# Performance work log

Hardware: AMD Instinct MI355X
Metric: run time of the kernel (lower is better)

Reference implementation:

```python
import jax, jax.numpy as jnp
import numpy as np
from jax import lax

HMA = 8.0
H = W = 34
A = 15
IMH = IMW = 270.0
AW = jnp.array([9.232984,16.0,27.712813,18.465969,32.0,55.425626,36.931937,64.0,110.851252,73.863875,128.0,221.702503,147.72775,256.0,443.405007], jnp.float32)
AH = jnp.array([27.72668,16.0,9.237604,55.453359,32.0,18.475209,110.906719,64.0,36.950417,221.813438,128.0,73.900834,443.626876,256.0,147.801669], jnp.float32)
RPN_MEAN = jnp.array([0.000437,0.002586,-0.123953,-0.081469], jnp.float32)
RPN_STD = jnp.array([0.12677,0.095741,0.3173,0.281042], jnp.float32)
RCNN_STD = jnp.array([0.1,0.1,0.2,0.2], jnp.float32)
RPN_MIN = 6.16056
RCNN_MIN = 8.8008
NUM_CLASS = 3

def _decode(t, acx, acy, aw, ah):
    cx = t[..., 0] * aw + acx
    cy = t[..., 1] * ah + acy
    bw = jnp.exp(t[..., 2]) * aw
    bh = jnp.exp(t[..., 3]) * ah
    x1 = jnp.clip(cx - 0.5 * (bw - 1.0), 0.0, IMW - 1.0)
    y1 = jnp.clip(cy - 0.5 * (bh - 1.0), 0.0, IMH - 1.0)
    x2 = jnp.clip(cx + 0.5 * (bw - 1.0), 0.0, IMW - 1.0)
    y2 = jnp.clip(cy + 0.5 * (bh - 1.0), 0.0, IMH - 1.0)
    return jnp.stack([x1, y1, x2, y2], -1)

def _nms(boxes, scores, thresh, top_n):
    # greedy hard NMS, fixed top_n output with validity mask
    x1, y1, x2, y2 = boxes[:, 0], boxes[:, 1], boxes[:, 2], boxes[:, 3]
    areas = (x2 - x1 + 1.0) * (y2 - y1 + 1.0)
    n = boxes.shape[0]
    def step(scur, _):
        j = jnp.argmax(scur)
        valid = scur[j] > 0.0
        bj = boxes[j]
        iw = jnp.maximum(jnp.minimum(x2, bj[2]) - jnp.maximum(x1, bj[0]) + 1.0, 0.0)
        ih = jnp.maximum(jnp.minimum(y2, bj[3]) - jnp.maximum(y1, bj[1]) + 1.0, 0.0)
        inter = iw * ih
        iou = inter / (areas + areas[j] - inter)
        sup = (iou > thresh) | (jnp.arange(n) == j)
        return jnp.where(sup, -1.0, scur), (j, valid)
    _, (idx, valid) = lax.scan(step, scores, None, length=top_n)
    return idx, valid

def _psroi_one(ftr, roi):
    # ftr: [10,7,7,H,W] position-sensitive features; roi: [x1,y1,x2,y2] image coords
    sw = roi[0] / HMA; sh = roi[1] / HMA
    ew = (roi[2] + 1.0) / HMA; eh = (roi[3] + 1.0) / HMA
    rh = jnp.maximum(eh - sh, 0.1); rw = jnp.maximum(ew - sw, 0.1)
    bh = rh / 7.0; bw = rw / 7.0
    g = jnp.arange(7, dtype=jnp.float32); s = jnp.arange(4, dtype=jnp.float32)
    ys = sh + g[:, None] * bh + (s[None, :] + 0.5) * (bh / 4.0)  # [7(ph),4]
    xs = sw + g[:, None] * bw + (s[None, :] + 0.5) * (bw / 4.0)  # [7(pw),4]
    y0 = jnp.floor(ys); x0 = jnp.floor(xs)
    dy = ys - y0; dx = xs - x0
    y0i = y0.astype(jnp.int32); x0i = x0.astype(jnp.int32)
    c = jnp.arange(10)[:, None, None, None, None]
    P = jnp.arange(7)[None, :, None, None, None]
    Q = jnp.arange(7)[None, None, :, None, None]
    def corner(yi, xi, wy, wx):
        my = ((yi >= 0) & (yi < H)).astype(jnp.float32)
        mx = ((xi >= 0) & (xi < W)).astype(jnp.float32)
        yc = jnp.clip(yi, 0, H - 1); xc = jnp.clip(xi, 0, W - 1)
        v = ftr[c, P, Q, yc[None, :, None, :, None], xc[None, None, :, None, :]]
        return v * (wy * my)[None, :, None, :, None] * (wx * mx)[None, None, :, None, :]
    val = (corner(y0i, x0i, 1 - dy, 1 - dx) + corner(y0i, x0i + 1, 1 - dy, dx)
         + corner(y0i + 1, x0i, dy, 1 - dx) + corner(y0i + 1, x0i + 1, dy, dx))
    return val.mean(axis=(3, 4))  # [10,7,7]

def reference(rpn_cls_prob_reshape, rpn_bbox_pred, ft_add_left_right, W_inner, b_inner, W_cls, b_cls, W_bbox, b_bbox):
    # ---------- RPNProposalSSD ----------
    fg = rpn_cls_prob_reshape[0, A:, :, :].reshape(-1)  # [A*H*W] fg probs
    t = rpn_bbox_pred[0].reshape(A, 4, H, W).transpose(0, 2, 3, 1)  # [A,H,W,4]
    t = t * RPN_STD + RPN_MEAN
    acx = (jnp.arange(W, dtype=jnp.float32) * HMA)[None, None, :]
    acy = (jnp.arange(H, dtype=jnp.float32) * HMA)[None, :, None]
    boxes = _decode(t, acx, acy, AW[:, None, None], AH[:, None, None]).reshape(-1, 4)
    bw = boxes[:, 2] - boxes[:, 0] + 1.0; bh = boxes[:, 3] - boxes[:, 1] + 1.0
    keep = (fg >= 0.2) & ((bw >= RPN_MIN) | (bh >= RPN_MIN))
    top_s, top_i = lax.top_k(jnp.where(keep, fg, -1.0), 3000)
    cand = boxes[top_i]
    idx, valid = _nms(cand, top_s, 0.7, 300)
    vm = valid.astype(jnp.float32)[:, None]
    rois_xy = cand[idx] * vm  # [300,4], padded rows zeroed
    rois = jnp.concatenate([jnp.zeros((300, 1), jnp.float32), rois_xy], axis=1)
    rpn_scores = top_s[idx][:, None] * vm  # [300,1]
    # ---------- DFMBPSROIAlign ----------
    ftr = ft_add_left_right[0].reshape(10, 7, 7, H, W)
    pooled = jax.vmap(lambda r: _psroi_one(ftr, r))(rois_xy)  # [300,10,7,7]
    # ---------- FC head ----------
    feat = jax.nn.relu(pooled.reshape(-1, 490) @ W_inner.T + b_inner)
    probs = jax.nn.softmax(feat @ W_cls.T + b_cls, axis=1)  # [300,4]
    bpred = feat @ W_bbox.T + b_bbox  # [300,16]
    # ---------- RCNNProposal ----------
    rw = rois_xy[:, 2] - rois_xy[:, 0] + 1.0; rh2 = rois_xy[:, 3] - rois_xy[:, 1] + 1.0
    rcx = rois_xy[:, 0] + 0.5 * (rw - 1.0); rcy = rois_xy[:, 1] + 0.5 * (rh2 - 1.0)
    obj_ok = (1.0 - probs[:, 0]) >= 0.1
    all_b, all_s, all_l, all_k = [], [], [], []
    for cidx in range(1, NUM_CLASS + 1):
        tc = bpred[:, 4 * cidx:4 * cidx + 4] * RCNN_STD  # rcnn mean is 0
        db = _decode(tc, rcx, rcy, rw, rh2)
        dw = db[:, 2] - db[:, 0] + 1.0; dh = db[:, 3] - db[:, 1] + 1.0
        sc = probs[:, cidx]
        k = valid & obj_ok & (sc >= 0.1) & ((dw >= RCNN_MIN) | (dh >= RCNN_MIN))
        all_b.append(db); all_s.append(sc)
        all_l.append(jnp.full((300,), float(cidx), jnp.float32)); all_k.append(k)
    cb = jnp.concatenate(all_b); cs = jnp.concatenate(all_s)
    cl = jnp.concatenate(all_l); ck = jnp.concatenate(all_k)
    ts2, ti2 = lax.top_k(jnp.where(ck, cs, -1.0), 300)
    cand2 = cb[ti2]; lab2 = cl[ti2]
    idx2, val2 = _nms(cand2, ts2, 0.5, 5)
    v2 = val2.astype(jnp.float32)
    bboxes = jnp.concatenate([cand2[idx2] * v2[:, None], (ts2[idx2] * v2)[:, None], (lab2[idx2] * v2)[:, None]], axis=1)  # [5,6] x1,y1,x2,y2,score,label
    return bboxes, rois, rpn_scores

def setup_inputs() -> dict:
    key = jax.random.key(0)
    ks = jax.random.split(key, 6)
    return {
        'rpn_cls_prob_reshape': jax.random.uniform(ks[0], (1, 2 * A, H, W), jnp.float32),
        'rpn_bbox_pred': jax.random.normal(ks[1], (1, 4 * A, H, W), jnp.float32) * 0.5,
        'ft_add_left_right': jax.random.normal(ks[2], (1, 490, H, W), jnp.float32),
        'W_inner': jax.random.normal(ks[3], (2048, 490), jnp.float32) * 0.02,
        'b_inner': jnp.zeros((2048,), jnp.float32),
        'W_cls': jax.random.normal(ks[4], (4, 2048), jnp.float32) * 0.02,
        'b_cls': jnp.zeros((4,), jnp.float32),
        'W_bbox': jax.random.normal(ks[5], (16, 2048), jnp.float32) * 0.02,
        'b_bbox': jnp.zeros((16,), jnp.float32),
    }
```

## Files before the change

kernel.cpp:

```cpp
#include <hip/hip_runtime.h>

#define NB 17340
#define TOPK1 3000
#define TOPK2 300
#define PTS 304

__constant__ float c_AW[15] = {9.232984, 16.0, 27.712813, 18.465969, 32.0, 55.425626,
                               36.931937, 64.0, 110.851252, 73.863875, 128.0, 221.702503,
                               147.72775, 256.0, 443.405007};
__constant__ float c_AH[15] = {27.72668, 16.0, 9.237604, 55.453359, 32.0, 18.475209,
                               110.906719, 64.0, 36.950417, 221.813438, 128.0, 73.900834,
                               443.626876, 256.0, 147.801669};

__device__ __forceinline__ unsigned mapf(float f) {
  unsigned u = __float_as_uint(f);
  return (u & 0x80000000u) ? ~u : (u | 0x80000000u);
}
__device__ __forceinline__ float unmapf(unsigned m) {
  unsigned u = (m & 0x80000000u) ? (m & 0x7FFFFFFFu) : ~m;
  return __uint_as_float(u);
}
__device__ __forceinline__ float clipc(float v) {
  return fminf(fmaxf(v, 0.0f), 269.0f);
}
__device__ __forceinline__ unsigned long long readlane64(unsigned long long v, int lane) {
  unsigned lo = (unsigned)__builtin_amdgcn_readlane((int)(unsigned)v, lane);
  unsigned hi = (unsigned)__builtin_amdgcn_readlane((int)(unsigned)(v >> 32), lane);
  return ((unsigned long long)hi << 32) | lo;
}

__global__ void k_decode(const float* __restrict__ cls, const float* __restrict__ pred,
                         float* __restrict__ boxes, float* __restrict__ scores,
                         unsigned int* __restrict__ hist) {
  int i = blockIdx.x * 256 + threadIdx.x;
  if (i >= NB) return;
  int a = i / 1156;
  int rem = i - a * 1156;
  int y = rem / 34;
  int x = rem - y * 34;
  float fg = cls[(15 + a) * 1156 + rem];
  const float* p = pred + a * 4 * 1156 + rem;
  float t0 = p[0]    * (float)0.12677  + (float)0.000437;
  float t1 = p[1156] * (float)0.095741 + (float)0.002586;
  float t2 = p[2312] * (float)0.3173   + (float)-0.123953;
  float t3 = p[3468] * (float)0.281042 + (float)-0.081469;
  float aw = c_AW[a], ah = c_AH[a];
  float cx = t0 * aw + (float)x * 8.0f;
  float cy = t1 * ah + (float)y * 8.0f;
  float bw = expf(t2) * aw;
  float bh = expf(t3) * ah;
  float x1 = clipc(cx - 0.5f * (bw - 1.0f));
  float y1 = clipc(cy - 0.5f * (bh - 1.0f));
  float x2 = clipc(cx + 0.5f * (bw - 1.0f));
  float y2 = clipc(cy + 0.5f * (bh - 1.0f));
  boxes[i * 4 + 0] = x1;
  boxes[i * 4 + 1] = y1;
  boxes[i * 4 + 2] = x2;
  boxes[i * 4 + 3] = y2;
  float w2 = x2 - x1 + 1.0f, h2 = y2 - y1 + 1.0f;
  bool keep = (fg >= 0.2f) && ((w2 >= (float)6.16056) || (h2 >= (float)6.16056));
  scores[i] = keep ? fg : -1.0f;
  if (keep) atomicAdd(&hist[mapf(fg) >> 18], 1u);
}

__global__ __launch_bounds__(256) void k_cutoff(const unsigned int* __restrict__ hist,
                                                unsigned int* __restrict__ bcut) {
  const int t = threadIdx.x;
  __shared__ unsigned int sh[16384];
  __shared__ unsigned int coarse[256];
  for (int i = t; i < 16384; i += 256) sh[i] = hist[i];
  __syncthreads();
  {
    unsigned s = 0;
    int b0 = t * 64;
    for (int b = 0; b < 64; ++b) s += sh[b0 + b];
    coarse[t] = s;
  }
  __syncthreads();
  if (t == 0) {
    unsigned acc = 0, nbefore = 0;
    int C = 0;
    for (int c = 255; c >= 0; --c) {
      if (acc + coarse[c] >= (unsigned)TOPK1) { C = c; nbefore = acc; break; }
      acc += coarse[c];
    }
    unsigned acc2 = nbefore;
    int B = C * 64;
    for (int b = C * 64 + 63; b >= C * 64; --b) {
      if (acc2 + sh[b] >= (unsigned)TOPK1) { B = b; break; }
      acc2 += sh[b];
    }
    bcut[0] = (unsigned)B;
  }
}

__global__ __launch_bounds__(256) void k_compact(const float* __restrict__ scores,
                                                 const unsigned int* __restrict__ bcut,
                                                 unsigned int* __restrict__ cnt,
                                                 unsigned long long* __restrict__ keys) {
  int i = blockIdx.x * 256 + threadIdx.x;
  const unsigned B = bcut[0];
  if (i < NB) {
    unsigned m = mapf(scores[i]);
    if ((m >> 18) >= B) {
      unsigned p = atomicAdd(cnt, 1u);
      if (p < 4096u) keys[p] = ((unsigned long long)m << 15) | (unsigned)(32767 - i);
    }
  }
}

__global__ __launch_bounds__(256) void k_sort(const float* __restrict__ boxes,
                                              const unsigned int* __restrict__ cnt,
                                              const unsigned long long* __restrict__ keys,
                                              unsigned int* __restrict__ sscore,
                                              float4* __restrict__ sbox) {
  const int t = threadIdx.x;
  __shared__ unsigned long long lk[4096];
  const int K = min((int)cnt[0], 4096);
  for (int i = t; i < 4096; i += 256) lk[i] = (i < K) ? keys[i] : 0ull;
  __syncthreads();
  int p = blockIdx.x * 32 + (t >> 3);
  const int s = t & 7;
  if (p < K) {
    unsigned long long kp = lk[p];
    int r = 0;
    for (int q = s; q < 4096; q += 64) {
#pragma unroll
      for (int u = 0; u < 8; ++u) r += (lk[q + 8 * u] > kp) ? 1 : 0;
    }
    r += __shfl_xor(r, 1);
    r += __shfl_xor(r, 2);
    r += __shfl_xor(r, 4);
    if (s == 0 && r < TOPK1) {
      int idx = 32767 - (int)(kp & 32767ull);
      sscore[r] = (unsigned)(kp >> 15);
      sbox[r] = ((const float4*)boxes)[idx];
    }
  }
}

__global__ __launch_bounds__(64) void k_iou(const float4* __restrict__ sbox,
                                            unsigned long long* __restrict__ mat) {
  const int wi = blockIdx.x, wj = blockIdx.y;
  if (wj < wi) return;
  __shared__ float4 cb[64];
  __shared__ float car[64];
  const int l = threadIdx.x;
  float4 c = sbox[wj * 64 + l];
  cb[l] = c;
  car[l] = (c.z - c.x + 1.0f) * (c.w - c.y + 1.0f);
  __syncthreads();
  const int ri = wi * 64 + l;
  float4 r = sbox[ri];
  float rar = (r.z - r.x + 1.0f) * (r.w - r.y + 1.0f);
  unsigned long long m = 0ull;
#pragma unroll 16
  for (int j = 0; j < 64; ++j) {
    float4 cc = cb[j];
    float iw = fmaxf(fminf(r.z, cc.z) - fmaxf(r.x, cc.x) + 1.0f, 0.0f);
    float ih = fmaxf(fminf(r.w, cc.w) - fmaxf(r.y, cc.y) + 1.0f, 0.0f);
    float inter = iw * ih;
    float iou = inter / (car[j] + rar - inter);
    if (iou > 0.7f) m |= (1ull << j);
  }
  mat[ri * 48 + wj] = m;
}

__global__ __launch_bounds__(256) void k_nms1(const unsigned int* __restrict__ sscore,
                                              const float4* __restrict__ sbox,
                                              const unsigned long long* __restrict__ mat,
                                              float* __restrict__ dout,
                                              float* __restrict__ rois_xy,
                                              float* __restrict__ validf) {
  const int t = threadIdx.x;
  __shared__ unsigned long long rowbuf[2][64][48];
  __shared__ unsigned int sc[3008];
  __shared__ int arank[300];
  __shared__ int s_A;
  for (int i = t; i < 3008; i += 256) sc[i] = (i < TOPK1) ? sscore[i] : 0u;
  if (t == 0) s_A = 0;

  {
    unsigned long long r0v[12];
#pragma unroll
    for (int i = 0; i < 12; ++i) r0v[i] = mat[t + 256 * i];
#pragma unroll
    for (int i = 0; i < 12; ++i) {
      int idx = t + 256 * i;
      rowbuf[0][idx / 48][idx % 48] = r0v[i];
    }
  }
  unsigned long long rgA[16], rgB[16];
  const int st = t - 64;
  if (t >= 64) {
#pragma unroll
    for (int i = 0; i < 16; ++i) rgA[i] = mat[1 * 3072 + st + 192 * i];
#pragma unroll
    for (int i = 0; i < 16; ++i) rgB[i] = mat[2 * 3072 + st + 192 * i];
  }
  __syncthreads();

  unsigned long long run = 0ull;
  int A = 0;
  const int l = t & 63;
  const int lw = (l < 48) ? l : 0;
  for (int c = 0; c < 47; ++c) {
    if (t < 64) {
      const bool okw = (l >= c) && (l < 47);
      unsigned long long supw = readlane64(run, c);
      bool aliveb = (sc[c * 64 + l] > 0x80000000u) && !((supw >> l) & 1ull);
      unsigned long long alive = __ballot(aliveb);
      int Aw = A;
      const int buf = c & 1;
      while (alive != 0ull && Aw < 300) {
        int j1 = __ffsll((long long)alive) - 1;
        unsigned long long rest = alive & (alive - 1ull);
        int j2 = (rest != 0ull) ? (__ffsll((long long)rest) - 1) : -1;
        unsigned long long v1 = rowbuf[buf][j1][lw];
        unsigned long long v2 = rowbuf[buf][(j2 >= 0 ? j2 : j1)][lw];
        if (l == 0) arank[Aw] = c * 64 + j1;
        Aw++;
        unsigned long long kill1 = readlane64(v1, c);
        run |= okw ? v1 : 0ull;
        alive &= ~kill1;
        if (j2 >= 0 && ((alive >> j2) & 1ull) && Aw < 300) {
          if (l == 0) arank[Aw] = c * 64 + j2;
          Aw++;
          unsigned long long kill2 = readlane64(v2, c);
          run |= okw ? v2 : 0ull;
          alive &= ~kill2;
        }
      }
      A = Aw;
      if (l == 0) s_A = Aw;
    } else if (c < 46) {
      int nb = (c + 1) & 1;
      if (((c + 1) & 1) == 1) {
#pragma unroll
        for (int i = 0; i < 16; ++i) {
          int idx = st + 192 * i;
          rowbuf[nb][idx / 48][idx % 48] = rgA[i];
        }
        if (c + 3 <= 46) {
#pragma unroll
          for (int i = 0; i < 16; ++i) rgA[i] = mat[(c + 3) * 3072 + st + 192 * i];
        }
      } else {
#pragma unroll
        for (int i = 0; i < 16; ++i) {
          int idx = st + 192 * i;
          rowbuf[nb][idx / 48][idx % 48] = rgB[i];
        }
        if (c + 3 <= 46) {
#pragma unroll
          for (int i = 0; i < 16; ++i) rgB[i] = mat[(c + 3) * 3072 + st + 192 * i];
        }
      }
    }
    __syncthreads();
    A = s_A;
    if (A >= 300) break;
    if (c < 46 && sc[(c + 1) * 64] <= 0x80000000u) break;
  }
  for (int a = t; a < A; a += 256) {
    int rk = arank[a];
    float4 b = sbox[rk];
    dout[30 + a * 5 + 0] = 0.0f;
    dout[30 + a * 5 + 1] = b.x;
    dout[30 + a * 5 + 2] = b.y;
    dout[30 + a * 5 + 3] = b.z;
    dout[30 + a * 5 + 4] = b.w;
    dout[1530 + a] = unmapf(sc[rk]);
    rois_xy[a * 4 + 0] = b.x; rois_xy[a * 4 + 1] = b.y;
    rois_xy[a * 4 + 2] = b.z; rois_xy[a * 4 + 3] = b.w;
    validf[a] = 1.0f;
  }
  for (int z = 30 + A * 5 + t; z < 1530; z += 256) dout[z] = 0.f;
  for (int z = 1530 + A + t; z < 1830; z += 256) dout[z] = 0.f;
  for (int z = A * 4 + t; z < 1200; z += 256) rois_xy[z] = 0.f;
  for (int z = A + t; z < 300; z += 256) validf[z] = 0.f;
}

__global__ __launch_bounds__(256) void k_psroi(const float* __restrict__ ft,
                                               const float* __restrict__ rois_xy,
                                               float* __restrict__ pooledT) {
  int r = blockIdx.x;
  __shared__ int2 ycs[28];
  __shared__ float2 wys[28];
  __shared__ int2 xcs[28];
  __shared__ float2 wxs[28];
  float r0 = rois_xy[r * 4 + 0], r1 = rois_xy[r * 4 + 1];
  float r2 = rois_xy[r * 4 + 2], r3 = rois_xy[r * 4 + 3];
  float sw = r0 * 0.125f;
  float sh = r1 * 0.125f;
  float ew = (r2 + 1.0f) * 0.125f;
  float eh = (r3 + 1.0f) * 0.125f;
  float rh = fmaxf(eh - sh, 0.1f);
  float rw = fmaxf(ew - sw, 0.1f);
  float bh = rh / 7.0f;
  float bwd = rw / 7.0f;
  const int t = threadIdx.x;
  if (t < 28) {
    int p = t >> 2, sy = t & 3;
    float ys = sh + (float)p * bh + ((float)sy + 0.5f) * (bh * 0.25f);
    float y0f = floorf(ys);
    float dy = ys - y0f;
    int y0 = (int)y0f;
    float wy0 = (1.0f - dy) * ((y0 >= 0 && y0 < 34) ? 1.f : 0.f);
    float wy1 = dy * ((y0 + 1 >= 0 && y0 + 1 < 34) ? 1.f : 0.f);
    ycs[t] = make_int2(min(max(y0, 0), 33), min(max(y0 + 1, 0), 33));
    wys[t] = make_float2(wy0, wy1);
  } else if (t >= 32 && t < 60) {
    int q = (t - 32) >> 2, sx = (t - 32) & 3;
    float xs = sw + (float)q * bwd + ((float)sx + 0.5f) * (bwd * 0.25f);
    float x0f = floorf(xs);
    float dx = xs - x0f;
    int x0 = (int)x0f;
    float wx0 = (1.0f - dx) * ((x0 >= 0 && x0 < 34) ? 1.f : 0.f);
    float wx1 = dx * ((x0 + 1 >= 0 && x0 + 1 < 34) ? 1.f : 0.f);
    xcs[t - 32] = make_int2(min(max(x0, 0), 33), min(max(x0 + 1, 0), 33));
    wxs[t - 32] = make_float2(wx0, wx1);
  }
  __syncthreads();
  for (int o = t; o < 490; o += 256) {
    int pq = o % 49;
    int p = pq / 7, q = pq - p * 7;
    const float* base = ft + o * 1156;
    float acc = 0.f;
#pragma unroll
    for (int sy = 0; sy < 4; ++sy) {
      int2 yc = ycs[p * 4 + sy];
      float2 wy = wys[p * 4 + sy];
#pragma unroll
      for (int sx = 0; sx < 4; ++sx) {
        int2 xc = xcs[q * 4 + sx];
        float2 wx = wxs[q * 4 + sx];
        float v00 = base[yc.x * 34 + xc.x], v01 = base[yc.x * 34 + xc.y];
        float v10 = base[yc.y * 34 + xc.x], v11 = base[yc.y * 34 + xc.y];
        acc += wy.x * wx.x * v00 + wy.x * wx.y * v01 + wy.y * wx.x * v10 + wy.y * wx.y * v11;
      }
    }
    pooledT[o * PTS + r] = acc * (1.0f / 16.0f);
  }
}

__global__ __launch_bounds__(256) void k_fc1(const float* __restrict__ pooledT,
                                             const float* __restrict__ Wi,
                                             const float* __restrict__ bi,
                                             float* __restrict__ feat) {
  __shared__ float As[2][32][68];
  __shared__ float Bs[2][32][68];
  const int t = threadIdx.x;
  const int tr = t >> 4, tc = t & 15;
  const int b = blockIdx.x;
  const int xcd = b & 7, s = b >> 3;
  const int r0 = (s % 5) * 64;
  const int o0 = (xcd + 8 * (s / 5)) * 64;
  float acc[4][4];
#pragma unroll
  for (int i = 0; i < 4; ++i)
#pragma unroll
    for (int j = 0; j < 4; ++j) acc[i][j] = 0.f;
  float ra[8], rb[8];

#pragma unroll
  for (int i = 0; i < 8; ++i) {
    int idx = t + 256 * i;
    int kk = idx >> 6, rr = idx & 63;
    ra[i] = (kk < 490 && r0 + rr < 300) ? pooledT[kk * PTS + r0 + rr] : 0.f;
    int oo = idx >> 5, k2 = idx & 31;
    rb[i] = Wi[(o0 + oo) * 490 + k2];
  }
#pragma unroll
  for (int i = 0; i < 8; ++i) {
    int idx = t + 256 * i;
    As[0][idx >> 6][idx & 63] = ra[i];
    Bs[0][idx & 31][idx >> 5] = rb[i];
  }
  __syncthreads();

  int cur = 0;
  for (int step = 0; step < 16; ++step) {
    if (step < 15) {
      int k0n = (step + 1) * 32;
#pragma unroll
      for (int i = 0; i < 8; ++i) {
        int idx = t + 256 * i;
        int kk = idx >> 6, rr = idx & 63;
        int k = k0n + kk;
        ra[i] = (k < 490 && r0 + rr < 300) ? pooledT[k * PTS + r0 + rr] : 0.f;
        int oo = idx >> 5, k2 = k0n + (idx & 31);
        rb[i] = (k2 < 490) ? Wi[(o0 + oo) * 490 + k2] : 0.f;
      }
    }
#pragma unroll
    for (int kk = 0; kk < 32; ++kk) {
      float4 a4 = *(const float4*)&As[cur][kk][tr * 4];
      float4 b4 = *(const float4*)&Bs[cur][kk][tc * 4];
      acc[0][0] += a4.x * b4.x; acc[0][1] += a4.x * b4.y; acc[0][2] += a4.x * b4.z; acc[0][3] += a4.x * b4.w;
      acc[1][0] += a4.y * b4.x; acc[1][1] += a4.y * b4.y; acc[1][2] += a4.y * b4.z; acc[1][3] += a4.y * b4.w;
      acc[2][0] += a4.z * b4.x; acc[2][1] += a4.z * b4.y; acc[2][2] += a4.z * b4.z; acc[2][3] += a4.z * b4.w;
      acc[3][0] += a4.w * b4.x; acc[3][1] += a4.w * b4.y; acc[3][2] += a4.w * b4.z; acc[3][3] += a4.w * b4.w;
    }
    __syncthreads();
    if (step < 15) {
      int nxt = cur ^ 1;
#pragma unroll
      for (int i = 0; i < 8; ++i) {
        int idx = t + 256 * i;
        As[nxt][idx >> 6][idx & 63] = ra[i];
        Bs[nxt][idx & 31][idx >> 5] = rb[i];
      }
      __syncthreads();
      cur = nxt;
    }
  }
  float4 bias = *(const float4*)&bi[o0 + tc * 4];
#pragma unroll
  for (int i = 0; i < 4; ++i) {
    int r = r0 + tr * 4 + i;
    if (r < 300) {
      float4 v;
      v.x = fmaxf(acc[i][0] + bias.x, 0.f);
      v.y = fmaxf(acc[i][1] + bias.y, 0.f);
      v.z = fmaxf(acc[i][2] + bias.z, 0.f);
      v.w = fmaxf(acc[i][3] + bias.w, 0.f);
      *(float4*)&feat[r * 2048 + o0 + tc * 4] = v;
    }
  }
}

__global__ __launch_bounds__(256) void k_fc2(const float* __restrict__ feat,
                                             const float* __restrict__ Wc,
                                             const float* __restrict__ bc,
                                             const float* __restrict__ Wb,
                                             const float* __restrict__ bb,
                                             const float* __restrict__ rois_xy,
                                             const float* __restrict__ validf,
                                             float* __restrict__ db2,
                                             float* __restrict__ msc2) {
  int r = blockIdx.x;
  int t = threadIdx.x;
  int l = t & 63, w = t >> 6;
  __shared__ float frow[2048];
  __shared__ float s_logit[20];
  __shared__ float s_probs[4];
  for (int i = t; i < 512; i += 256)
    ((float4*)frow)[i] = ((const float4*)(feat + r * 2048))[i];
  __syncthreads();
  for (int o = w; o < 20; o += 4) {
    const float* wr = (o < 4) ? (Wc + o * 2048) : (Wb + (o - 4) * 2048);
    float p = 0.f;
#pragma unroll
    for (int j = 0; j < 8; ++j) {
      float4 wv = ((const float4*)wr)[l + 64 * j];
      float4 fv = ((const float4*)frow)[l + 64 * j];
      p += wv.x * fv.x + wv.y * fv.y + wv.z * fv.z + wv.w * fv.w;
    }
    for (int off = 32; off > 0; off >>= 1) p += __shfl_xor(p, off);
    if (l == 0) s_logit[o] = p + ((o < 4) ? bc[o] : bb[o - 4]);
  }
  __syncthreads();
  if (t == 0) {
    float m = fmaxf(fmaxf(s_logit[0], s_logit[1]), fmaxf(s_logit[2], s_logit[3]));
    float e0 = expf(s_logit[0] - m), e1 = expf(s_logit[1] - m);
    float e2 = expf(s_logit[2] - m), e3 = expf(s_logit[3] - m);
    float ssum = e0 + e1 + e2 + e3;
    s_probs[0] = e0 / ssum; s_probs[1] = e1 / ssum;
    s_probs[2] = e2 / ssum; s_probs[3] = e3 / ssum;
  }
  __syncthreads();
  if (t < 3) {
    int c = t + 1;
    float x1 = rois_xy[r * 4 + 0], y1 = rois_xy[r * 4 + 1];
    float x2 = rois_xy[r * 4 + 2], y2 = rois_xy[r * 4 + 3];
    float rwv = x2 - x1 + 1.0f, rhv = y2 - y1 + 1.0f;
    float rcx = x1 + 0.5f * (rwv - 1.0f), rcy = y1 + 0.5f * (rhv - 1.0f);
    float t0 = s_logit[4 + 4 * c + 0] * 0.1f;
    float t1 = s_logit[4 + 4 * c + 1] * 0.1f;
    float t2 = s_logit[4 + 4 * c + 2] * 0.2f;
    float t3 = s_logit[4 + 4 * c + 3] * 0.2f;
    float cx = t0 * rwv + rcx, cy = t1 * rhv + rcy;
    float bw = expf(t2) * rwv, bh = expf(t3) * rhv;
    float dx1 = clipc(cx - 0.5f * (bw - 1.0f));
    float dy1 = clipc(cy - 0.5f * (bh - 1.0f));
    float dx2 = clipc(cx + 0.5f * (bw - 1.0f));
    float dy2 = clipc(cy + 0.5f * (bh - 1.0f));
    float dw = dx2 - dx1 + 1.0f, dh = dy2 - dy1 + 1.0f;
    float sc = s_probs[c];
    bool objok = (1.0f - s_probs[0]) >= 0.1f;
    bool valid = validf[r] > 0.5f;
    bool kf = valid && objok && (sc >= 0.1f) && ((dw >= (float)8.8008) || (dh >= (float)8.8008));
    int i2 = (c - 1) * 300 + r;
    db2[i2 * 4 + 0] = dx1; db2[i2 * 4 + 1] = dy1;
    db2[i2 * 4 + 2] = dx2; db2[i2 * 4 + 3] = dy2;
    msc2[i2] = kf ? sc : -1.0f;
  }
}

__global__ __launch_bounds__(1024) void k_nms2(const float* __restrict__ db2,
                                               const float* __restrict__ msc2,
                                               float* __restrict__ dout) {
  const int t = threadIdx.x;
  __shared__ unsigned long long lk[1024];
  __shared__ unsigned long long sk[1024];
  __shared__ float4 abox[5];
  __shared__ float aar[5];
  __shared__ int s_A;
  sk[t] = 0ull;
  lk[t] = (t < 900) ? (((unsigned long long)mapf(msc2[t]) << 10) | (unsigned)(1023 - t)) : 0ull;
  if (t == 0) s_A = 0;
  __syncthreads();
  if (t < 900) {
    unsigned long long kp = lk[t];
    int r = 0;
#pragma unroll 8
    for (int q = 0; q < 1024; ++q) r += (lk[q] > kp) ? 1 : 0;
    sk[r] = kp;
  }
  __syncthreads();
  if (t < 64) {
    int A = 0;
    for (int base = 0; base < TOPK2 && A < 5; base += 64) {
      unsigned headm = (unsigned)(sk[base] >> 10);
      if (headm <= 0x80000000u) break;
      int rank = base + t;
      unsigned long long key = sk[rank];
      unsigned mk = (unsigned)(key >> 10);
      bool active = (rank < TOPK2) && (mk > 0x80000000u);
      int idx = 1023 - (int)(key & 1023ull);
      float4 bx = make_float4(0.f, 0.f, 0.f, 0.f);
      float area = 0.f;
      if (active) {
        bx = ((const float4*)db2)[idx];
        area = (bx.z - bx.x + 1.0f) * (bx.w - bx.y + 1.0f);
      }
      bool alive = active;
      for (int a = 0; a < A; ++a) {
        float4 ab = abox[a];
        float iw = fmaxf(fminf(bx.z, ab.z) - fmaxf(bx.x, ab.x) + 1.0f, 0.0f);
        float ih = fmaxf(fminf(bx.w, ab.w) - fmaxf(bx.y, ab.y) + 1.0f, 0.0f);
        float inter = iw * ih;
        float iou = inter / (area + aar[a] - inter);
        if (iou > 0.5f) { alive = false; break; }
      }
      unsigned long long bal = __ballot(alive);
      while (bal != 0ull && A < 5) {
        int j = __ffsll((long long)bal) - 1;
        float jx1 = __shfl(bx.x, j), jy1 = __shfl(bx.y, j);
        float jx2 = __shfl(bx.z, j), jy2 = __shfl(bx.w, j);
        float jar = __shfl(area, j);
        if (t == j) {
          abox[A] = bx; aar[A] = area;
          dout[A * 6 + 0] = bx.x; dout[A * 6 + 1] = bx.y;
          dout[A * 6 + 2] = bx.z; dout[A * 6 + 3] = bx.w;
          dout[A * 6 + 4] = unmapf(mk);
          dout[A * 6 + 5] = (float)(idx / 300 + 1);
        }
        if (alive) {
          float iw = fmaxf(fminf(bx.z, jx2) - fmaxf(bx.x, jx1) + 1.0f, 0.0f);
          float ih = fmaxf(fminf(bx.w, jy2) - fmaxf(bx.y, jy1) + 1.0f, 0.0f);
          float inter = iw * ih;
          float iou = inter / (area + jar - inter);
          if (iou > 0.5f || t == j) alive = false;
        }
        A++;
        bal = __ballot(alive);
      }
    }
    if (t == 0) s_A = A;
  }
  __syncthreads();
  int A = s_A;
  for (int z = A * 6 + t; z < 30; z += 1024) dout[z] = 0.f;
}

extern "C" void kernel_launch(void* const* d_in, const int* in_sizes, int n_in,
                              void* d_out, int out_size, void* d_ws, size_t ws_size,
                              hipStream_t stream) {
  const float* cls  = (const float*)d_in[0];
  const float* pred = (const float*)d_in[1];
  const float* ft   = (const float*)d_in[2];
  const float* Wi   = (const float*)d_in[3];
  const float* bi   = (const float*)d_in[4];
  const float* Wc   = (const float*)d_in[5];
  const float* bc   = (const float*)d_in[6];
  const float* Wb   = (const float*)d_in[7];
  const float* bb   = (const float*)d_in[8];
  float* out = (float*)d_out;
  float* w = (float*)d_ws;
  float* boxes   = w;
  float* scores  = w + 69360;
  unsigned int* hist = (unsigned int*)(w + 86700);
  unsigned int* cnt  = (unsigned int*)(w + 103084);
  unsigned int* bcut = (unsigned int*)(w + 103085);
  unsigned long long* keys = (unsigned long long*)(w + 103088);
  unsigned int* sscore = (unsigned int*)(w + 111280);
  float4* sbox   = (float4*)(w + 114280);
  float* rois_xy = w + 126312;
  float* validf  = w + 127512;
  float* pooledT = w + 127812;
  float* feat    = w + 276772;
  unsigned long long* mat = (unsigned long long*)(w + 276772);
  float* db2     = w + 891172;
  float* msc2    = w + 894772;

  hipMemsetAsync(hist, 0, 16385 * sizeof(unsigned int), stream);
  k_decode<<<68, 256, 0, stream>>>(cls, pred, boxes, scores, hist);
  k_cutoff<<<1, 256, 0, stream>>>(hist, bcut);
  k_compact<<<68, 256, 0, stream>>>(scores, bcut, cnt, keys);
  k_sort<<<128, 256, 0, stream>>>(boxes, cnt, keys, sscore, sbox);
  k_iou<<<dim3(47, 47), 64, 0, stream>>>(sbox, mat);
  k_nms1<<<1, 256, 0, stream>>>(sscore, sbox, mat, out, rois_xy, validf);
  k_psroi<<<300, 256, 0, stream>>>(ft, rois_xy, pooledT);
  k_fc1<<<160, 256, 0, stream>>>(pooledT, Wi, bi, feat);
  k_fc2<<<300, 256, 0, stream>>>(feat, Wc, bc, Wb, bb, rois_xy, validf, db2, msc2);
  k_nms2<<<1, 1024, 0, stream>>>(db2, msc2, out);
}
```

Measured before the change: 198.1 us.

## Split NMS chunk into intra-block diagonal pass and batched row OR; halve fc1 tile

Inside each 64-box chunk of the greedy NMS, survivors are now chosen first using only the diagonal suppression word, read once per lane. After that the full suppression rows of the kept boxes are ORed into the running mask four at a time. This takes the wide row loads off the serial dependency chain. The fc1 GEMM output tile is halved from 64 to 32 columns so the grid doubles to 320 blocks for better CU occupancy, and one __syncthreads per k-step is removed. The cost is more redundant A-tile loads and lower arithmetic intensity per block.

```diff
diff --git a/kernel.cpp b/kernel.cpp
--- a/kernel.cpp
+++ b/kernel.cpp
@@ -207,29 +207,39 @@
   for (int c = 0; c < 47; ++c) {
     if (t < 64) {
       const bool okw = (l >= c) && (l < 47);
+      const int buf = c & 1;
+      unsigned long long diag = rowbuf[buf][l][c];
       unsigned long long supw = readlane64(run, c);
       bool aliveb = (sc[c * 64 + l] > 0x80000000u) && !((supw >> l) & 1ull);
       unsigned long long alive = __ballot(aliveb);
+      unsigned long long accm = 0ull;
       int Aw = A;
-      const int buf = c & 1;
       while (alive != 0ull && Aw < 300) {
-        int j1 = __ffsll((long long)alive) - 1;
-        unsigned long long rest = alive & (alive - 1ull);
-        int j2 = (rest != 0ull) ? (__ffsll((long long)rest) - 1) : -1;
+        int j = __ffsll((long long)alive) - 1;
+        if (l == 0) arank[Aw] = c * 64 + j;
+        Aw++;
+        accm |= (1ull << j);
+        unsigned long long kill = readlane64(diag, j);
+        alive &= ~kill;
+      }
+      while (accm != 0ull) {
+        int j1 = __ffsll((long long)accm) - 1;
+        unsigned long long m2 = accm & (accm - 1ull);
+        int j2 = (m2 != 0ull) ? (__ffsll((long long)m2) - 1) : j1;
+        unsigned long long m3 = (m2 != 0ull) ? (m2 & (m2 - 1ull)) : 0ull;
+        int j3 = (m3 != 0ull) ? (__ffsll((long long)m3) - 1) : j1;
+        unsigned long long m4 = (m3 != 0ull) ? (m3 & (m3 - 1ull)) : 0ull;
+        int j4 = (m4 != 0ull) ? (__ffsll((long long)m4) - 1) : j1;
         unsigned long long v1 = rowbuf[buf][j1][lw];
-        unsigned long long v2 = rowbuf[buf][(j2 >= 0 ? j2 : j1)][lw];
-        if (l == 0) arank[Aw] = c * 64 + j1;
-        Aw++;
-        unsigned long long kill1 = readlane64(v1, c);
-        run |= okw ? v1 : 0ull;
-        alive &= ~kill1;
-        if (j2 >= 0 && ((alive >> j2) & 1ull) && Aw < 300) {
-          if (l == 0) arank[Aw] = c * 64 + j2;
-          Aw++;
-          unsigned long long kill2 = readlane64(v2, c);
-          run |= okw ? v2 : 0ull;
-          alive &= ~kill2;
-        }
+        unsigned long long v2 = rowbuf[buf][j2][lw];
+        unsigned long long v3 = rowbuf[buf][j3][lw];
+        unsigned long long v4 = rowbuf[buf][j4][lw];
+        unsigned long long o = v1;
+        if (m2 != 0ull) o |= v2;
+        if (m3 != 0ull) o |= v3;
+        if (m4 != 0ull) o |= v4;
+        if (okw) run |= o;
+        accm = (m4 != 0ull) ? (m4 & (m4 - 1ull)) : 0ull;
       }
       A = Aw;
       if (l == 0) s_A = Aw;
@@ -349,25 +359,27 @@
                                              const float* __restrict__ bi,
                                              float* __restrict__ feat) {
   __shared__ float As[2][32][68];
-  __shared__ float Bs[2][32][68];
+  __shared__ float Bs[2][32][36];
   const int t = threadIdx.x;
   const int tr = t >> 4, tc = t & 15;
   const int b = blockIdx.x;
   const int xcd = b & 7, s = b >> 3;
   const int r0 = (s % 5) * 64;
-  const int o0 = (xcd + 8 * (s / 5)) * 64;
-  float acc[4][4];
-#pragma unroll
-  for (int i = 0; i < 4; ++i)
-#pragma unroll
-    for (int j = 0; j < 4; ++j) acc[i][j] = 0.f;
-  float ra[8], rb[8];
+  const int o0 = (xcd + 8 * (s / 5)) * 32;
+  float acc[4][2];
+#pragma unroll
+  for (int i = 0; i < 4; ++i) { acc[i][0] = 0.f; acc[i][1] = 0.f; }
+  float ra[8], rb[4];
 
 #pragma unroll
   for (int i = 0; i < 8; ++i) {
     int idx = t + 256 * i;
     int kk = idx >> 6, rr = idx & 63;
     ra[i] = (kk < 490 && r0 + rr < 300) ? pooledT[kk * PTS + r0 + rr] : 0.f;
+  }
+#pragma unroll
+  for (int i = 0; i < 4; ++i) {
+    int idx = t + 256 * i;
     int oo = idx >> 5, k2 = idx & 31;
     rb[i] = Wi[(o0 + oo) * 490 + k2];
   }
@@ -375,6 +387,10 @@
   for (int i = 0; i < 8; ++i) {
     int idx = t + 256 * i;
     As[0][idx >> 6][idx & 63] = ra[i];
+  }
+#pragma unroll
+  for (int i = 0; i < 4; ++i) {
+    int idx = t + 256 * i;
     Bs[0][idx & 31][idx >> 5] = rb[i];
   }
   __syncthreads();
@@ -389,6 +405,10 @@
         int kk = idx >> 6, rr = idx & 63;
         int k = k0n + kk;
         ra[i] = (k < 490 && r0 + rr < 300) ? pooledT[k * PTS + r0 + rr] : 0.f;
+      }
+#pragma unroll
+      for (int i = 0; i < 4; ++i) {
+        int idx = t + 256 * i;
         int oo = idx >> 5, k2 = k0n + (idx & 31);
         rb[i] = (k2 < 490) ? Wi[(o0 + oo) * 490 + k2] : 0.f;
       }
@@ -396,36 +416,37 @@
 #pragma unroll
     for (int kk = 0; kk < 32; ++kk) {
       float4 a4 = *(const float4*)&As[cur][kk][tr * 4];
-      float4 b4 = *(const float4*)&Bs[cur][kk][tc * 4];
-      acc[0][0] += a4.x * b4.x; acc[0][1] += a4.x * b4.y; acc[0][2] += a4.x * b4.z; acc[0][3] += a4.x * b4.w;
-      acc[1][0] += a4.y * b4.x; acc[1][1] += a4.y * b4.y; acc[1][2] += a4.y * b4.z; acc[1][3] += a4.y * b4.w;
-      acc[2][0] += a4.z * b4.x; acc[2][1] += a4.z * b4.y; acc[2][2] += a4.z * b4.z; acc[2][3] += a4.z * b4.w;
-      acc[3][0] += a4.w * b4.x; acc[3][1] += a4.w * b4.y; acc[3][2] += a4.w * b4.z; acc[3][3] += a4.w * b4.w;
-    }
-    __syncthreads();
+      float2 b2 = *(const float2*)&Bs[cur][kk][tc * 2];
+      acc[0][0] += a4.x * b2.x; acc[0][1] += a4.x * b2.y;
+      acc[1][0] += a4.y * b2.x; acc[1][1] += a4.y * b2.y;
+      acc[2][0] += a4.z * b2.x; acc[2][1] += a4.z * b2.y;
+      acc[3][0] += a4.w * b2.x; acc[3][1] += a4.w * b2.y;
+    }
     if (step < 15) {
       int nxt = cur ^ 1;
 #pragma unroll
       for (int i = 0; i < 8; ++i) {
         int idx = t + 256 * i;
         As[nxt][idx >> 6][idx & 63] = ra[i];
+      }
+#pragma unroll
+      for (int i = 0; i < 4; ++i) {
+        int idx = t + 256 * i;
         Bs[nxt][idx & 31][idx >> 5] = rb[i];
       }
-      __syncthreads();
       cur = nxt;
     }
-  }
-  float4 bias = *(const float4*)&bi[o0 + tc * 4];
+    __syncthreads();
+  }
+  float2 bias = *(const float2*)&bi[o0 + tc * 2];
 #pragma unroll
   for (int i = 0; i < 4; ++i) {
     int r = r0 + tr * 4 + i;
     if (r < 300) {
-      float4 v;
+      float2 v;
       v.x = fmaxf(acc[i][0] + bias.x, 0.f);
       v.y = fmaxf(acc[i][1] + bias.y, 0.f);
-      v.z = fmaxf(acc[i][2] + bias.z, 0.f);
-      v.w = fmaxf(acc[i][3] + bias.w, 0.f);
-      *(float4*)&feat[r * 2048 + o0 + tc * 4] = v;
+      *(float2*)&feat[r * 2048 + o0 + tc * 2] = v;
     }
   }
 }
@@ -613,7 +634,7 @@
   k_iou<<<dim3(47, 47), 64, 0, stream>>>(sbox, mat);
   k_nms1<<<1, 256, 0, stream>>>(sscore, sbox, mat, out, rois_xy, validf);
   k_psroi<<<300, 256, 0, stream>>>(ft, rois_xy, pooledT);
-  k_fc1<<<160, 256, 0, stream>>>(pooledT, Wi, bi, feat);
+  k_fc1<<<320, 256, 0, stream>>>(pooledT, Wi, bi, feat);
   k_fc2<<<300, 256, 0, stream>>>(feat, Wc, bc, Wb, bb, rois_xy, validf, db2, msc2);
   k_nms2<<<1, 1024, 0, stream>>>(db2, msc2, out);
 }
```

Result: slower. 204.7 us (+3.3%).
